# Optimization experiments

Hardware: AMD Instinct MI355X
Metric: run time of the kernel (lower is better)

The kernel has to match this reference:

```python
import jax, jax.numpy as jnp
import numpy as np

B, N, C = 2, 2048, 1024
H = 16
D = C // H  # 64 head_dim
SCALE = D ** -0.5


def setup_inputs() -> dict:
    key = jax.random.key(0)
    k1, k2, k3 = jax.random.split(key, 3)
    x = jax.random.normal(k1, (B, N, C), dtype=jnp.float32)
    w_qkv = jax.random.normal(k2, (C, 3 * C), dtype=jnp.float32) * (C ** -0.5)
    w_proj = jax.random.normal(k3, (C, C), dtype=jnp.float32) * (C ** -0.5)
    b_proj = jnp.zeros((C,), dtype=jnp.float32)
    return {"x": x, "w_qkv": w_qkv, "w_proj": w_proj, "b_proj": b_proj}


def reference(x, w_qkv, w_proj, b_proj):
    # qkv projection (no bias, qkv_bias=False)
    qkv = x @ w_qkv                                   # [B,N,3C]
    qkv = qkv.reshape(B, N, 3, H, D)
    qkv = jnp.transpose(qkv, (2, 0, 3, 1, 4))         # [3,B,H,N,D]
    q, k, v = qkv[0], qkv[1], qkv[2]
    # scaled dot-product attention (full softmax == chunked loop in original)
    scores = jnp.einsum('bhqd,bhkd->bhqk', q, k) * SCALE
    attn = jax.nn.softmax(scores, axis=-1)
    out = jnp.einsum('bhqk,bhkd->bhqd', attn, v)      # [B,H,N,D]
    out = jnp.transpose(out, (0, 2, 1, 3)).reshape(B, N, C)
    return out @ w_proj + b_proj
```

## Files before the change

### kernel.cpp

```cpp
#include <hip/hip_runtime.h>
#include <stdint.h>

typedef float f32x4 __attribute__((ext_vector_type(4)));
typedef float f32x16 __attribute__((ext_vector_type(16)));
typedef __bf16 bf16x8 __attribute__((ext_vector_type(8)));
typedef unsigned int u32x4 __attribute__((ext_vector_type(4)));
typedef unsigned short u16x4 __attribute__((ext_vector_type(4)));

#define DEV __device__ __forceinline__

#define QSCALE_LOG2E 0.18033688011112042f

DEV unsigned short f2bf(float f) {
    unsigned u = __builtin_bit_cast(unsigned, f);
    u += 0x7fffu + ((u >> 16) & 1u);
    return (unsigned short)(u >> 16);
}

DEV unsigned pack2bf(float a, float b) {
    unsigned short ua = __builtin_bit_cast(unsigned short, (__bf16)a);
    unsigned short ub = __builtin_bit_cast(unsigned short, (__bf16)b);
    return (unsigned)ua | ((unsigned)ub << 16);
}

DEV void pswap(unsigned& a, unsigned& b) {
    asm volatile("v_permlane32_swap_b32 %0, %1" : "+v"(a), "+v"(b));
}

DEV void gload16(const void* g, void* l) {
    __builtin_amdgcn_global_load_lds(
        (const __attribute__((address_space(1))) unsigned int*)(uintptr_t)g,
        (__attribute__((address_space(3))) unsigned int*)(unsigned int)(uintptr_t)l,
        16, 0, 0);
}

__global__ void k_cvt(const float* __restrict__ in, unsigned short* __restrict__ out, int n4) {
    int i = blockIdx.x * 256 + threadIdx.x;
    int st = gridDim.x * 256;
    for (; i < n4; i += st) {
        f32x4 v = *(const f32x4*)(in + (size_t)i * 4);
        u16x4 o;
        o[0] = f2bf(v[0]); o[1] = f2bf(v[1]); o[2] = f2bf(v[2]); o[3] = f2bf(v[3]);
        *(u16x4*)(out + (size_t)i * 4) = o;
    }
}

__global__ void k_transpose(const float* __restrict__ in, unsigned short* __restrict__ out, int Nc) {
    __shared__ unsigned short tl[64][68];
    int n0 = blockIdx.x * 64, k0 = blockIdx.y * 64;
#pragma unroll
    for (int i = 0; i < 16; i++) {
        int idx = i * 256 + threadIdx.x;
        int kr = idx >> 6, nc = idx & 63;
        tl[kr][nc] = f2bf(in[(size_t)(k0 + kr) * Nc + n0 + nc]);
    }
    __syncthreads();
#pragma unroll
    for (int i = 0; i < 8; i++) {
        int idx = i * 256 + threadIdx.x;
        int nr = idx >> 5, kp2 = idx & 31;
        unsigned vv = (unsigned)tl[kp2 * 2][nr] | ((unsigned)tl[kp2 * 2 + 1][nr] << 16);
        *(unsigned*)(out + (size_t)(n0 + nr) * 1024 + k0 + kp2 * 2) = vv;
    }
}

template <int MODE>
__global__ __launch_bounds__(256) void k_gemm(
    const unsigned short* __restrict__ A, const unsigned short* __restrict__ Bt, int K,
    unsigned short* __restrict__ q, unsigned short* __restrict__ kk_,
    unsigned short* __restrict__ vT, const float* __restrict__ bias,
    float* __restrict__ outf) {
    __shared__ unsigned short As[2][128 * 64];
    __shared__ unsigned short Bs[2][128 * 64];
    const int tid = threadIdx.x;
    const int w = tid >> 6, l = tid & 63, g = l >> 4, lr = l & 15;
    const int wr = w >> 1, wc = w & 1;
    const int nwg = gridDim.x * gridDim.y, cpx = nwg >> 3;
    const int lin = blockIdx.y * gridDim.x + blockIdx.x;
    const int swz = (lin & 7) * cpx + (lin >> 3);
    const int m0 = (swz / gridDim.x) * 128, n0 = (swz % gridDim.x) * 128;
    f32x4 acc[4][4] = {};

    auto STAGE = [&](int buf, int k0) {
#pragma unroll
        for (int i = 0; i < 4; i++) {
            int c = i * 256 + tid;
            gload16(A + (size_t)(m0 + (c >> 3)) * K + k0 + (c & 7) * 8, (char*)As[buf] + c * 16);
            gload16(Bt + (size_t)(n0 + (c >> 3)) * K + k0 + (c & 7) * 8, (char*)Bs[buf] + c * 16);
        }
    };

    STAGE(0, 0);
    asm volatile("s_waitcnt vmcnt(0)" ::: "memory");
    __builtin_amdgcn_s_barrier();
    __builtin_amdgcn_sched_barrier(0);

    int cur = 0;
    for (int k0 = 0; k0 < K; k0 += 64) {
        if (k0 + 64 < K) STAGE(cur ^ 1, k0 + 64);
        const unsigned short* Ac = As[cur];
        const unsigned short* Bc = Bs[cur];
#pragma unroll
        for (int kk = 0; kk < 2; kk++) {
            bf16x8 af[4], bfv[4];
#pragma unroll
            for (int mi = 0; mi < 4; mi++)
                af[mi] = *(const bf16x8*)(Ac + (wr * 64 + mi * 16 + lr) * 64 + kk * 32 + g * 8);
#pragma unroll
            for (int ni = 0; ni < 4; ni++)
                bfv[ni] = *(const bf16x8*)(Bc + (wc * 64 + ni * 16 + lr) * 64 + kk * 32 + g * 8);
#pragma unroll
            for (int mi = 0; mi < 4; mi++)
#pragma unroll
                for (int ni = 0; ni < 4; ni++)
                    acc[mi][ni] = __builtin_amdgcn_mfma_f32_16x16x32_bf16(af[mi], bfv[ni], acc[mi][ni], 0, 0, 0);
        }
        asm volatile("s_waitcnt vmcnt(0)" ::: "memory");
        __builtin_amdgcn_s_barrier();
        __builtin_amdgcn_sched_barrier(0);
        cur ^= 1;
    }

#pragma unroll
    for (int mi = 0; mi < 4; mi++) {
#pragma unroll
        for (int ni = 0; ni < 4; ni++) {
            if (MODE == 1) {
                int row0 = m0 + wr * 64 + mi * 16 + g * 4;
                int col = n0 + wc * 64 + ni * 16 + lr;
                int b = row0 >> 11, nn = row0 & 2047;
                int which = col >> 10, cc = col & 1023;
                int h = cc >> 6, d = cc & 63;
                if (which == 2) {
                    u16x4 pv;
#pragma unroll
                    for (int r = 0; r < 4; r++) pv[r] = f2bf(acc[mi][ni][r]);
                    *(u16x4*)&vT[((size_t)(b * 16 + h) * 64 + d) * 2048 + nn] = pv;
                } else {
                    unsigned short* dst = (which == 0) ? q : kk_;
                    const float sc = (which == 0) ? QSCALE_LOG2E : 1.f;
#pragma unroll
                    for (int r = 0; r < 4; r++)
                        dst[((size_t)(b * 16 + h) * 2048 + nn + r) * 64 + d] = f2bf(acc[mi][ni][r] * sc);
                }
            } else {
#pragma unroll
                for (int r = 0; r < 4; r++) {
                    int row = m0 + wr * 64 + mi * 16 + g * 4 + r;
                    int col = n0 + wc * 64 + ni * 16 + lr;
                    outf[(size_t)row * 1024 + col] = acc[mi][ni][r] + bias[col];
                }
            }
        }
    }
}

__global__ __launch_bounds__(512, 4) void k_attn(
    const unsigned short* __restrict__ qb, const unsigned short* __restrict__ kb,
    const unsigned short* __restrict__ vTb, unsigned short* __restrict__ ao) {
    __shared__ __align__(16) char smem[65536];
    const int tid = threadIdx.x;
    const int w = tid >> 6, l = tid & 63, l31 = l & 31, hf = l >> 5;
    const int qg = w & 3, kvh = w >> 2;
    const int bid = blockIdx.x;
    const int xcd = bid & 7, slot = bid >> 3;
    const int bh = xcd * 4 + (slot >> 4), qb_ = slot & 15;
    const int b = bh >> 4, h = bh & 15;
    const unsigned short* qp = qb + (size_t)bh * 131072;
    const unsigned short* kp = kb + (size_t)bh * 131072 + (size_t)kvh * 65536;
    const unsigned short* vTp = vTb + (size_t)bh * 131072 + kvh * 1024;

    const int qrow = qb_ * 128 + qg * 32 + l31;
    bf16x8 qf[4];
#pragma unroll
    for (int dc = 0; dc < 4; dc++)
        qf[dc] = *(const bf16x8*)(qp + (size_t)qrow * 64 + dc * 16 + hf * 8);
    asm volatile("s_waitcnt vmcnt(0)" ::: "memory");

    f32x16 o_acc[2] = {};
    float l_r = 0.f;

    const int sr8 = l >> 3;
    const int sco = ((l & 7) ^ sr8) * 8;
    char* sbase = smem + kvh * 32768;
    auto STAGE = [&](char* dst, int kv0) {
#pragma unroll
        for (int i = 0; i < 2; i++) {
            int r = qg + 4 * i;
            gload16(kp + (size_t)(kv0 + r * 8 + sr8) * 64 + sco, dst + r * 1024 + (size_t)l * 16);
            gload16(vTp + (size_t)(r * 8 + sr8) * 2048 + kv0 + sco, dst + 8192 + r * 1024 + (size_t)l * 16);
        }
    };

    STAGE(sbase, 0);
    asm volatile("s_waitcnt vmcnt(0)" ::: "memory");
    __builtin_amdgcn_s_barrier();
    __builtin_amdgcn_sched_barrier(0);

    const int lb = l31 & 7;
    int cur = 0;
    for (int t = 0; t < 16; ++t) {
        if (t < 15) STAGE(sbase + (cur ^ 1) * 16384, (t + 1) * 64);
        const char* p0 = sbase + cur * 16384;

        f32x16 s[2] = {};
        __builtin_amdgcn_s_setprio(1);
#pragma unroll
        for (int kt = 0; kt < 2; kt++)
#pragma unroll
            for (int dc = 0; dc < 4; dc++) {
                bf16x8 kf = *(const bf16x8*)(p0 + (kt * 32 + l31) * 128 + (((2 * dc + hf) ^ lb) * 16));
                s[kt] = __builtin_amdgcn_mfma_f32_32x32x16_bf16(kf, qf[dc], s[kt], 0, 0, 0);
            }
        __builtin_amdgcn_s_setprio(0);

        float s0 = 0.f, s1 = 0.f, s2 = 0.f, s3 = 0.f;
#pragma unroll
        for (int kt = 0; kt < 2; kt++)
#pragma unroll
            for (int r = 0; r < 16; r += 4) {
                float e0 = __builtin_amdgcn_exp2f(s[kt][r]);
                float e1 = __builtin_amdgcn_exp2f(s[kt][r + 1]);
                float e2 = __builtin_amdgcn_exp2f(s[kt][r + 2]);
                float e3 = __builtin_amdgcn_exp2f(s[kt][r + 3]);
                s[kt][r] = e0; s[kt][r + 1] = e1; s[kt][r + 2] = e2; s[kt][r + 3] = e3;
                s0 += e0; s1 += e1; s2 += e2; s3 += e3;
            }
        float ssum = (s0 + s1) + (s2 + s3);
        ssum += __shfl_xor(ssum, 32);
        l_r += ssum;

        bf16x8 pf[4];
#pragma unroll
        for (int kt = 0; kt < 2; kt++) {
            unsigned wd[8];
#pragma unroll
            for (int i = 0; i < 8; i++) wd[i] = pack2bf(s[kt][2 * i], s[kt][2 * i + 1]);
#pragma unroll
            for (int cl = 0; cl < 2; cl++) {
                unsigned b0 = wd[4 * cl + 0], b2 = wd[4 * cl + 2];
                unsigned b1 = wd[4 * cl + 1], b3 = wd[4 * cl + 3];
                pswap(b0, b2);
                pswap(b1, b3);
                u32x4 bw; bw[0] = b0; bw[1] = b1; bw[2] = b2; bw[3] = b3;
                pf[2 * kt + cl] = __builtin_bit_cast(bf16x8, bw);
            }
        }

        __builtin_amdgcn_s_setprio(1);
#pragma unroll
        for (int c4 = 0; c4 < 4; c4++)
#pragma unroll
            for (int dt = 0; dt < 2; dt++) {
                bf16x8 vf = *(const bf16x8*)(p0 + 8192 + (dt * 32 + l31) * 128 + (((2 * c4 + hf) ^ lb) * 16));
                o_acc[dt] = __builtin_amdgcn_mfma_f32_32x32x16_bf16(vf, pf[c4], o_acc[dt], 0, 0, 0);
            }
        __builtin_amdgcn_s_setprio(0);

        if (t < 15) {
            asm volatile("s_waitcnt vmcnt(0)" ::: "memory");
            __builtin_amdgcn_s_barrier();
            __builtin_amdgcn_sched_barrier(0);
        }
        cur ^= 1;
    }

    __syncthreads();
    float* dO = (float*)(smem + qg * 8704);
    float* dL = (float*)(smem + 34816 + qg * 256);
    if (kvh == 1) {
#pragma unroll
        for (int i = 0; i < 16; i++) dO[l * 34 + i] = o_acc[0][i];
#pragma unroll
        for (int i = 0; i < 16; i++) dO[l * 34 + 16 + i] = o_acc[1][i];
        dL[l] = l_r;
    }
    __syncthreads();
    if (kvh == 0) {
        float linv = 1.f / (l_r + dL[l]);
        unsigned short* aop = ao + ((size_t)b * 2048 + qrow) * 1024 + h * 64;
#pragma unroll
        for (int dt = 0; dt < 2; dt++)
#pragma unroll
            for (int rg = 0; rg < 4; rg++) {
                u16x4 pv;
#pragma unroll
                for (int k = 0; k < 4; k++) {
                    int r = rg * 4 + k;
                    pv[k] = f2bf((o_acc[dt][r] + dO[l * 34 + dt * 16 + r]) * linv);
                }
                *(u16x4*)(aop + 8 * rg + 4 * hf + 32 * dt) = pv;
            }
    }
}

extern "C" void kernel_launch(void* const* d_in, const int* in_sizes, int n_in,
                              void* d_out, int out_size, void* d_ws, size_t ws_size,
                              hipStream_t stream) {
    (void)in_sizes; (void)n_in; (void)out_size; (void)ws_size;
    const float* x      = (const float*)d_in[0];
    const float* w_qkv  = (const float*)d_in[1];
    const float* w_proj = (const float*)d_in[2];
    const float* b_proj = (const float*)d_in[3];
    float* out = (float*)d_out;
    char* ws = (char*)d_ws;

    unsigned short* xb     = (unsigned short*)(ws);
    unsigned short* ao     = (unsigned short*)(ws);
    unsigned short* wqkvT  = (unsigned short*)(ws + 8388608);
    unsigned short* wprojT = (unsigned short*)(ws + 14680064);
    unsigned short* qb     = (unsigned short*)(ws + 16777216);
    unsigned short* kb     = (unsigned short*)(ws + 25165824);
    unsigned short* vTb    = (unsigned short*)(ws + 33554432);

    k_cvt<<<2048, 256, 0, stream>>>(x, xb, 1048576);
    k_transpose<<<dim3(48, 16), 256, 0, stream>>>(w_qkv, wqkvT, 3072);
    k_transpose<<<dim3(16, 16), 256, 0, stream>>>(w_proj, wprojT, 1024);
    k_gemm<1><<<dim3(24, 32), 256, 0, stream>>>(xb, wqkvT, 1024, qb, kb, vTb, nullptr, nullptr);
    k_attn<<<512, 512, 0, stream>>>(qb, kb, vTb, ao);
    k_gemm<3><<<dim3(8, 32), 256, 0, stream>>>(ao, wprojT, 1024, nullptr, nullptr, nullptr, b_proj, out);
}
```

Baseline: 124.2 us.

## Process two 32-row Q tiles per wave to reuse staged K/V fragments

Each attention wave now handles two 32-row query tiles (256 rows per block) instead of one, so every K and V fragment read from LDS feeds two MFMAs. The grid drops from 512 to 256 blocks and the launch bound is relaxed to 2 blocks per CU to leave room for the doubled accumulators and Q registers. The cross-half reduction of the two KV halves is done per tile in a loop with a tighter LDS stride. This cuts LDS traffic and global K/V staging per query row, at the cost of higher register pressure, lower occupancy, and fewer blocks (256) spread over the CUs.

```diff
diff --git a/kernel.cpp b/kernel.cpp
--- a/kernel.cpp
+++ b/kernel.cpp
@@ -155,7 +155,7 @@
     }
 }
 
-__global__ __launch_bounds__(512, 4) void k_attn(
+__global__ __launch_bounds__(512, 2) void k_attn(
     const unsigned short* __restrict__ qb, const unsigned short* __restrict__ kb,
     const unsigned short* __restrict__ vTb, unsigned short* __restrict__ ao) {
     __shared__ __align__(16) char smem[65536];
@@ -164,21 +164,23 @@
     const int qg = w & 3, kvh = w >> 2;
     const int bid = blockIdx.x;
     const int xcd = bid & 7, slot = bid >> 3;
-    const int bh = xcd * 4 + (slot >> 4), qb_ = slot & 15;
+    const int bh = xcd * 4 + (slot >> 3), qb_ = slot & 7;
     const int b = bh >> 4, h = bh & 15;
     const unsigned short* qp = qb + (size_t)bh * 131072;
     const unsigned short* kp = kb + (size_t)bh * 131072 + (size_t)kvh * 65536;
     const unsigned short* vTp = vTb + (size_t)bh * 131072 + kvh * 1024;
 
-    const int qrow = qb_ * 128 + qg * 32 + l31;
-    bf16x8 qf[4];
-#pragma unroll
-    for (int dc = 0; dc < 4; dc++)
-        qf[dc] = *(const bf16x8*)(qp + (size_t)qrow * 64 + dc * 16 + hf * 8);
+    const int qrow0 = qb_ * 256 + qg * 64 + l31;
+    bf16x8 qf[2][4];
+#pragma unroll
+    for (int ti = 0; ti < 2; ti++)
+#pragma unroll
+        for (int dc = 0; dc < 4; dc++)
+            qf[ti][dc] = *(const bf16x8*)(qp + (size_t)(qrow0 + ti * 32) * 64 + dc * 16 + hf * 8);
     asm volatile("s_waitcnt vmcnt(0)" ::: "memory");
 
-    f32x16 o_acc[2] = {};
-    float l_r = 0.f;
+    f32x16 o_acc[2][2] = {};
+    float l_r[2] = {0.f, 0.f};
 
     const int sr8 = l >> 3;
     const int sco = ((l & 7) ^ sr8) * 8;
@@ -203,47 +205,52 @@
         if (t < 15) STAGE(sbase + (cur ^ 1) * 16384, (t + 1) * 64);
         const char* p0 = sbase + cur * 16384;
 
-        f32x16 s[2] = {};
+        f32x16 s[2][2] = {};
         __builtin_amdgcn_s_setprio(1);
 #pragma unroll
         for (int kt = 0; kt < 2; kt++)
 #pragma unroll
             for (int dc = 0; dc < 4; dc++) {
                 bf16x8 kf = *(const bf16x8*)(p0 + (kt * 32 + l31) * 128 + (((2 * dc + hf) ^ lb) * 16));
-                s[kt] = __builtin_amdgcn_mfma_f32_32x32x16_bf16(kf, qf[dc], s[kt], 0, 0, 0);
+                s[0][kt] = __builtin_amdgcn_mfma_f32_32x32x16_bf16(kf, qf[0][dc], s[0][kt], 0, 0, 0);
+                s[1][kt] = __builtin_amdgcn_mfma_f32_32x32x16_bf16(kf, qf[1][dc], s[1][kt], 0, 0, 0);
             }
         __builtin_amdgcn_s_setprio(0);
 
-        float s0 = 0.f, s1 = 0.f, s2 = 0.f, s3 = 0.f;
-#pragma unroll
-        for (int kt = 0; kt < 2; kt++)
-#pragma unroll
-            for (int r = 0; r < 16; r += 4) {
-                float e0 = __builtin_amdgcn_exp2f(s[kt][r]);
-                float e1 = __builtin_amdgcn_exp2f(s[kt][r + 1]);
-                float e2 = __builtin_amdgcn_exp2f(s[kt][r + 2]);
-                float e3 = __builtin_amdgcn_exp2f(s[kt][r + 3]);
-                s[kt][r] = e0; s[kt][r + 1] = e1; s[kt][r + 2] = e2; s[kt][r + 3] = e3;
-                s0 += e0; s1 += e1; s2 += e2; s3 += e3;
-            }
-        float ssum = (s0 + s1) + (s2 + s3);
-        ssum += __shfl_xor(ssum, 32);
-        l_r += ssum;
-
-        bf16x8 pf[4];
-#pragma unroll
-        for (int kt = 0; kt < 2; kt++) {
-            unsigned wd[8];
-#pragma unroll
-            for (int i = 0; i < 8; i++) wd[i] = pack2bf(s[kt][2 * i], s[kt][2 * i + 1]);
-#pragma unroll
-            for (int cl = 0; cl < 2; cl++) {
-                unsigned b0 = wd[4 * cl + 0], b2 = wd[4 * cl + 2];
-                unsigned b1 = wd[4 * cl + 1], b3 = wd[4 * cl + 3];
-                pswap(b0, b2);
-                pswap(b1, b3);
-                u32x4 bw; bw[0] = b0; bw[1] = b1; bw[2] = b2; bw[3] = b3;
-                pf[2 * kt + cl] = __builtin_bit_cast(bf16x8, bw);
+        bf16x8 pf[2][4];
+#pragma unroll
+        for (int ti = 0; ti < 2; ti++) {
+            float s0 = 0.f, s1 = 0.f, s2 = 0.f, s3 = 0.f;
+#pragma unroll
+            for (int kt = 0; kt < 2; kt++)
+#pragma unroll
+                for (int r = 0; r < 16; r += 4) {
+                    float e0 = __builtin_amdgcn_exp2f(s[ti][kt][r]);
+                    float e1 = __builtin_amdgcn_exp2f(s[ti][kt][r + 1]);
+                    float e2 = __builtin_amdgcn_exp2f(s[ti][kt][r + 2]);
+                    float e3 = __builtin_amdgcn_exp2f(s[ti][kt][r + 3]);
+                    s[ti][kt][r] = e0; s[ti][kt][r + 1] = e1;
+                    s[ti][kt][r + 2] = e2; s[ti][kt][r + 3] = e3;
+                    s0 += e0; s1 += e1; s2 += e2; s3 += e3;
+                }
+            float ssum = (s0 + s1) + (s2 + s3);
+            ssum += __shfl_xor(ssum, 32);
+            l_r[ti] += ssum;
+#pragma unroll
+            for (int kt = 0; kt < 2; kt++) {
+                unsigned wd[8];
+#pragma unroll
+                for (int i = 0; i < 8; i++)
+                    wd[i] = pack2bf(s[ti][kt][2 * i], s[ti][kt][2 * i + 1]);
+#pragma unroll
+                for (int cl = 0; cl < 2; cl++) {
+                    unsigned b0 = wd[4 * cl + 0], b2 = wd[4 * cl + 2];
+                    unsigned b1 = wd[4 * cl + 1], b3 = wd[4 * cl + 3];
+                    pswap(b0, b2);
+                    pswap(b1, b3);
+                    u32x4 bw; bw[0] = b0; bw[1] = b1; bw[2] = b2; bw[3] = b3;
+                    pf[ti][2 * kt + cl] = __builtin_bit_cast(bf16x8, bw);
+                }
             }
         }
 
@@ -253,7 +260,8 @@
 #pragma unroll
             for (int dt = 0; dt < 2; dt++) {
                 bf16x8 vf = *(const bf16x8*)(p0 + 8192 + (dt * 32 + l31) * 128 + (((2 * c4 + hf) ^ lb) * 16));
-                o_acc[dt] = __builtin_amdgcn_mfma_f32_32x32x16_bf16(vf, pf[c4], o_acc[dt], 0, 0, 0);
+                o_acc[0][dt] = __builtin_amdgcn_mfma_f32_32x32x16_bf16(vf, pf[0][c4], o_acc[0][dt], 0, 0, 0);
+                o_acc[1][dt] = __builtin_amdgcn_mfma_f32_32x32x16_bf16(vf, pf[1][c4], o_acc[1][dt], 0, 0, 0);
             }
         __builtin_amdgcn_s_setprio(0);
 
@@ -265,32 +273,35 @@
         cur ^= 1;
     }
 
-    __syncthreads();
-    float* dO = (float*)(smem + qg * 8704);
-    float* dL = (float*)(smem + 34816 + qg * 256);
-    if (kvh == 1) {
-#pragma unroll
-        for (int i = 0; i < 16; i++) dO[l * 34 + i] = o_acc[0][i];
-#pragma unroll
-        for (int i = 0; i < 16; i++) dO[l * 34 + 16 + i] = o_acc[1][i];
-        dL[l] = l_r;
-    }
-    __syncthreads();
-    if (kvh == 0) {
-        float linv = 1.f / (l_r + dL[l]);
-        unsigned short* aop = ao + ((size_t)b * 2048 + qrow) * 1024 + h * 64;
-#pragma unroll
-        for (int dt = 0; dt < 2; dt++)
-#pragma unroll
-            for (int rg = 0; rg < 4; rg++) {
-                u16x4 pv;
-#pragma unroll
-                for (int k = 0; k < 4; k++) {
-                    int r = rg * 4 + k;
-                    pv[k] = f2bf((o_acc[dt][r] + dO[l * 34 + dt * 16 + r]) * linv);
-                }
-                *(u16x4*)(aop + 8 * rg + 4 * hf + 32 * dt) = pv;
-            }
+    float* dO = (float*)(smem + qg * 8448);
+    float* dL = (float*)(smem + 33792 + qg * 256);
+#pragma unroll
+    for (int ti = 0; ti < 2; ti++) {
+        __syncthreads();
+        if (kvh == 1) {
+#pragma unroll
+            for (int i = 0; i < 16; i++) dO[l * 33 + i] = o_acc[ti][0][i];
+#pragma unroll
+            for (int i = 0; i < 16; i++) dO[l * 33 + 16 + i] = o_acc[ti][1][i];
+            dL[l] = l_r[ti];
+        }
+        __syncthreads();
+        if (kvh == 0) {
+            float linv = 1.f / (l_r[ti] + dL[l]);
+            unsigned short* aop = ao + ((size_t)b * 2048 + qrow0 + ti * 32) * 1024 + h * 64;
+#pragma unroll
+            for (int dt = 0; dt < 2; dt++)
+#pragma unroll
+                for (int rg = 0; rg < 4; rg++) {
+                    u16x4 pv;
+#pragma unroll
+                    for (int k = 0; k < 4; k++) {
+                        int r = rg * 4 + k;
+                        pv[k] = f2bf((o_acc[ti][dt][r] + dO[l * 33 + dt * 16 + r]) * linv);
+                    }
+                    *(u16x4*)(aop + 8 * rg + 4 * hf + 32 * dt) = pv;
+                }
+        }
     }
 }
 
@@ -317,6 +328,6 @@
     k_transpose<<<dim3(48, 16), 256, 0, stream>>>(w_qkv, wqkvT, 3072);
     k_transpose<<<dim3(16, 16), 256, 0, stream>>>(w_proj, wprojT, 1024);
     k_gemm<1><<<dim3(24, 32), 256, 0, stream>>>(xb, wqkvT, 1024, qb, kb, vTb, nullptr, nullptr);
-    k_attn<<<512, 512, 0, stream>>>(qb, kb, vTb, ao);
+    k_attn<<<256, 512, 0, stream>>>(qb, kb, vTb, ao);
     k_gemm<3><<<dim3(8, 32), 256, 0, stream>>>(ao, wprojT, 1024, nullptr, nullptr, nullptr, b_proj, out);
 }
```

Result: faster. 120.0 us (-3.4%).
